# Optimization experiments

Hardware: AMD Instinct MI355X
Metric: run time of the kernel (lower is better)

## Reference

```python
import jax, jax.numpy as jnp
import numpy as np

NUM_HEADS = 16
D_K = 8  # == n_qubits


def setup_inputs() -> dict:
    key = jax.random.key(0)
    k1, k2, k3 = jax.random.split(key, 3)
    x = jax.random.normal(k1, (4, 2048, 128), dtype=jnp.float32)
    # trainable RX angles, one per qubit (tq.RX has_params=True)
    theta = jax.random.normal(k2, (D_K,), dtype=jnp.float32)
    # out_proj: Linear(embed_dim, embed_dim, bias=False)
    w_out = jax.random.normal(k3, (128, 128), dtype=jnp.float32) * (1.0 / np.sqrt(128.0))
    return {"x": x, "theta": theta, "w_out": w_out}


def quantum_features(x, theta):
    # x: [b, s, e]. Per head of size d_k: encode RX(x_i), trainable RX(theta_i)
    # (composes to RX(x_i + theta_i)), CNOT ladder [i, i+1], measure PauliZ.
    # Heisenberg picture: Z_w -> Z_0...Z_w, so <Z_w> = prod_{i<=w} cos(x_i + theta_i).
    b, s, e = x.shape
    heads = x.reshape(b, s, NUM_HEADS, D_K)
    return jnp.cumprod(jnp.cos(heads + theta), axis=-1)  # [b, s, h, d_k]


def reference(x, theta, w_out):
    b, s, e = x.shape
    # q == k == v: same shared q_layer applied to the same x three times.
    qkv = quantum_features(x, theta)            # [b, s, h, d_k]
    q = qkv.transpose(0, 2, 1, 3)               # [b, h, s, d_k]
    scores = jnp.einsum('bhqd,bhkd->bhqk', q, q) / np.sqrt(D_K)
    attn = jax.nn.softmax(scores, axis=-1)      # dropout is identity at eval
    out = jnp.einsum('bhqk,bhkd->bhqd', attn, q)
    out = out.transpose(0, 2, 1, 3).reshape(b, s, e)
    return out @ w_out.T
```

## Files before the change

kernel.cpp:

```cpp
#include <hip/hip_runtime.h>

#define BATCH 4
#define SEQ   2048
#define EMB   128
#define NH    16
#define DK    8

#define QSCALE 0.510069726f

typedef _Float16 v4h  __attribute__((ext_vector_type(4)));
typedef _Float16 v8h  __attribute__((ext_vector_type(8)));
typedef __fp16   v2fp __attribute__((ext_vector_type(2)));
typedef float    v4f  __attribute__((ext_vector_type(4)));
typedef float    v16f __attribute__((ext_vector_type(16)));

#define CHUNK  512
#define NCH    (SEQ / CHUNK)
#define VTP    520

__launch_bounds__(256, 4)
__global__ void attn_kernel(const float* __restrict__ x,
                            const float* __restrict__ theta,
                            _Float16* __restrict__ Ah ) {
  __shared__ __align__(16) _Float16 Kl[CHUNK * 8];
  __shared__ __align__(16) _Float16 VT[10][VTP];

  const int tid = threadIdx.x;
  const int L   = tid & 63;
  const int ln  = L & 31;
  const int hf  = L >> 5;
  const int wv  = tid >> 6;
  const int bh  = blockIdx.x >> 3;
  const int qg  = blockIdx.x & 7;
  const int b = bh >> 4;
  const int h = bh & 15;

  float th[DK];
#pragma unroll
  for (int i = 0; i < DK; ++i) th[i] = theta[i];

  for (int i = tid; i < VTP; i += 256) {
    VT[8][i] = (_Float16)1.0f;
    VT[9][i] = (_Float16)0.0f;
  }

  const int c0 = qg >> 1;
  const int mrow = (ln < 9) ? ln : 9;
  const float* xb = x + (size_t)b * SEQ * EMB + h * DK;

  float4 pa0, pa1, pb0, pb1;
  {
    const float* xp = xb + (size_t)(c0 * CHUNK + tid) * EMB;
    pa0 = *(const float4*)(xp);
    pa1 = *(const float4*)(xp + 4);
    pb0 = *(const float4*)(xp + 256 * EMB);
    pb1 = *(const float4*)(xp + 256 * EMB + 4);
  }

  v8h qf0 = {0, 0, 0, 0, 0, 0, 0, 0};
  v8h qf1 = {0, 0, 0, 0, 0, 0, 0, 0};
  v16f acc0, acc1, zf;
#pragma unroll
  for (int i = 0; i < 16; ++i) { acc0[i] = 0.f; acc1[i] = 0.f; zf[i] = 0.f; }

  for (int cc = 0; cc < NCH; ++cc) {
    if (cc) __syncthreads();

    {
      float r0[8], r1[8];
      r0[0] = __cosf(pa0.x + th[0]);
      r0[1] = r0[0] * __cosf(pa0.y + th[1]);
      r0[2] = r0[1] * __cosf(pa0.z + th[2]);
      r0[3] = r0[2] * __cosf(pa0.w + th[3]);
      r0[4] = r0[3] * __cosf(pa1.x + th[4]);
      r0[5] = r0[4] * __cosf(pa1.y + th[5]);
      r0[6] = r0[5] * __cosf(pa1.z + th[6]);
      r0[7] = r0[6] * __cosf(pa1.w + th[7]);
      r1[0] = __cosf(pb0.x + th[0]);
      r1[1] = r1[0] * __cosf(pb0.y + th[1]);
      r1[2] = r1[1] * __cosf(pb0.z + th[2]);
      r1[3] = r1[2] * __cosf(pb0.w + th[3]);
      r1[4] = r1[3] * __cosf(pb1.x + th[4]);
      r1[5] = r1[4] * __cosf(pb1.y + th[5]);
      r1[6] = r1[5] * __cosf(pb1.z + th[6]);
      r1[7] = r1[6] * __cosf(pb1.w + th[7]);

      _Float16 h0[8], h1[8];
#pragma unroll
      for (int i = 0; i < 8; ++i) { h0[i] = (_Float16)r0[i]; h1[i] = (_Float16)r1[i]; }

      union { v4h v[2]; float4 f; } u0, u1;
      u0.v[0] = (v4h){h0[0], h0[1], h0[2], h0[3]};
      u0.v[1] = (v4h){h0[4], h0[5], h0[6], h0[7]};
      u1.v[0] = (v4h){h1[0], h1[1], h1[2], h1[3]};
      u1.v[1] = (v4h){h1[4], h1[5], h1[6], h1[7]};
      *(float4*)&Kl[tid * 8]         = u0.f;
      *(float4*)&Kl[(tid + 256) * 8] = u1.f;

      const int j0 = tid, j1 = tid + 256;
      const int col0 = (j0 & ~15) | (j0 & 3) | ((j0 & 4) << 1) | ((j0 & 8) >> 1);
      const int col1 = (j1 & ~15) | (j1 & 3) | ((j1 & 4) << 1) | ((j1 & 8) >> 1);
#pragma unroll
      for (int d = 0; d < 8; ++d) {
        VT[d][col0] = h0[d];
        VT[d][col1] = h1[d];
      }
    }
    __syncthreads();

    if (cc + 1 < NCH) {
      const int cn = (c0 + cc + 1) & (NCH - 1);
      const float* xp = xb + (size_t)(cn * CHUNK + tid) * EMB;
      pa0 = *(const float4*)(xp);
      pa1 = *(const float4*)(xp + 4);
      pb0 = *(const float4*)(xp + 256 * EMB);
      pb1 = *(const float4*)(xp + 256 * EMB + 4);
    }

    if (cc == 0 && hf == 0) {
      const int ql = (qg & 1) * 256 + wv * 64 + ln;
      const _Float16 qs = (_Float16)QSCALE;
      const v8h qsc = {qs, qs, qs, qs, qs, qs, qs, qs};
      qf0 = *(const v8h*)&Kl[ql * 8] * qsc;
      qf1 = *(const v8h*)&Kl[(ql + 32) * 8] * qsc;
    }

    v8h kf = *(const v8h*)&Kl[ln * 8];
#pragma unroll 2
    for (int kb = 0; kb < CHUNK / 32; ++kb) {
      const v8h kf_n = *(const v8h*)&Kl[((((kb + 1) & 15) * 32) + ln) * 8];
      const v16f s0 = __builtin_amdgcn_mfma_f32_32x32x16_f16(kf, qf0, zf, 0, 0, 0);
      const v16f s1 = __builtin_amdgcn_mfma_f32_32x32x16_f16(kf, qf1, zf, 0, 0, 0);
      const v8h vt0 = *(const v8h*)&VT[mrow][kb * 32 + hf * 8];
      const v8h vt1 = *(const v8h*)&VT[mrow][kb * 32 + 16 + hf * 8];
      union { v2fp p[4]; v8h v; } a0, a1, b0, b1;
#pragma unroll
      for (int i = 0; i < 4; ++i) {
        a0.p[i] = __builtin_amdgcn_cvt_pkrtz(
            __builtin_amdgcn_exp2f(s0[2 * i]),
            __builtin_amdgcn_exp2f(s0[2 * i + 1]));
        a1.p[i] = __builtin_amdgcn_cvt_pkrtz(
            __builtin_amdgcn_exp2f(s0[8 + 2 * i]),
            __builtin_amdgcn_exp2f(s0[8 + 2 * i + 1]));
      }
      acc0 = __builtin_amdgcn_mfma_f32_32x32x16_f16(vt0, a0.v, acc0, 0, 0, 0);
      acc0 = __builtin_amdgcn_mfma_f32_32x32x16_f16(vt1, a1.v, acc0, 0, 0, 0);
#pragma unroll
      for (int i = 0; i < 4; ++i) {
        b0.p[i] = __builtin_amdgcn_cvt_pkrtz(
            __builtin_amdgcn_exp2f(s1[2 * i]),
            __builtin_amdgcn_exp2f(s1[2 * i + 1]));
        b1.p[i] = __builtin_amdgcn_cvt_pkrtz(
            __builtin_amdgcn_exp2f(s1[8 + 2 * i]),
            __builtin_amdgcn_exp2f(s1[8 + 2 * i + 1]));
      }
      acc1 = __builtin_amdgcn_mfma_f32_32x32x16_f16(vt0, b0.v, acc1, 0, 0, 0);
      acc1 = __builtin_amdgcn_mfma_f32_32x32x16_f16(vt1, b1.v, acc1, 0, 0, 0);
      kf = kf_n;
    }
  }

  {
    const int qrow0 = qg * 256 + wv * 64 + ln;
    const float den0 = __shfl(acc0[4], ln, 64);
    const float inv0 = 1.0f / den0;
    v4h o0 = {(_Float16)(acc0[0] * inv0), (_Float16)(acc0[1] * inv0),
              (_Float16)(acc0[2] * inv0), (_Float16)(acc0[3] * inv0)};
    *(v4h*)(Ah + ((size_t)b * SEQ + qrow0) * EMB + h * DK + hf * 4) = o0;

    const float den1 = __shfl(acc1[4], ln, 64);
    const float inv1 = 1.0f / den1;
    v4h o1 = {(_Float16)(acc1[0] * inv1), (_Float16)(acc1[1] * inv1),
              (_Float16)(acc1[2] * inv1), (_Float16)(acc1[3] * inv1)};
    *(v4h*)(Ah + ((size_t)b * SEQ + qrow0 + 32) * EMB + h * DK + hf * 4) = o1;
  }
}

__launch_bounds__(256, 4)
__global__ void proj_kernel(const _Float16* __restrict__ Ah,
                            const float* __restrict__ W,
                            float* __restrict__ out) {
  __shared__ __align__(16) _Float16 Ahs[32][136];
  __shared__ __align__(16) _Float16 Whs[64][136];

  const int tid  = threadIdx.x;
  const int L    = tid & 63;
  const int wv   = tid >> 6;
  const int quad = L >> 4;
  const int ln   = L & 15;
  const int rowbase = blockIdx.x * 32;
  const int colbase = blockIdx.y * 64;

#pragma unroll
  for (int it = 0; it < 2; ++it) {
    const int idx = it * 256 + tid;
    const int r  = idx >> 4;
    const int c8 = idx & 15;
    *(uint4*)&Ahs[r][c8 * 8] =
        *(const uint4*)(Ah + (size_t)(rowbase + r) * EMB + c8 * 8);
  }
#pragma unroll
  for (int it = 0; it < 8; ++it) {
    const int idx = it * 256 + tid;
    const int n  = idx >> 5;
    const int c4 = idx & 31;
    const float4 w = *(const float4*)(W + (size_t)(colbase + n) * EMB + c4 * 4);
    v4h wh = {(_Float16)w.x, (_Float16)w.y, (_Float16)w.z, (_Float16)w.w};
    *(v4h*)&Whs[n][c4 * 4] = wh;
  }
  __syncthreads();

  const int rowoff = (wv & 1) * 16;
  const int coloff = (wv >> 1) * 32;

  v4f acc[2];
#pragma unroll
  for (int nt = 0; nt < 2; ++nt) acc[nt] = (v4f){0.f, 0.f, 0.f, 0.f};

#pragma unroll
  for (int k8 = 0; k8 < 8; ++k8) {
    const v4h af = *(const v4h*)&Ahs[rowoff + ln][k8 * 16 + quad * 4];
#pragma unroll
    for (int nt = 0; nt < 2; ++nt) {
      const v4h bf = *(const v4h*)&Whs[coloff + nt * 16 + ln][k8 * 16 + quad * 4];
      acc[nt] = __builtin_amdgcn_mfma_f32_16x16x16f16(af, bf, acc[nt], 0, 0, 0);
    }
  }

#pragma unroll
  for (int nt = 0; nt < 2; ++nt) {
    const int col = colbase + coloff + nt * 16 + ln;
#pragma unroll
    for (int r = 0; r < 4; ++r) {
      out[(size_t)(rowbase + rowoff + quad * 4 + r) * EMB + col] = acc[nt][r];
    }
  }
}

extern "C" void kernel_launch(void* const* d_in, const int* in_sizes, int n_in,
                              void* d_out, int out_size, void* d_ws, size_t ws_size,
                              hipStream_t stream) {
  const float* x     = (const float*)d_in[0];
  const float* theta = (const float*)d_in[1];
  const float* w_out = (const float*)d_in[2];
  float* out = (float*)d_out;

  _Float16* Ah = (_Float16*)d_ws;

  attn_kernel<<<dim3(512), dim3(256), 0, stream>>>(x, theta, Ah);

  proj_kernel<<<dim3((BATCH * SEQ) / 32, 2), dim3(256), 0, stream>>>(Ah, w_out, out);
}
```

Measured before the change: 93.72 us.

## Fuse output projection into attention kernel via last-block-done counters

Merges the attention and projection kernels into one launch. Each attention block bumps an atomic counter for its (batch, query-group) tile, and the 16th block to arrive loads W into shared memory and computes the 256x128 projection for those rows from the fp16 attention output in global memory. This removes the second launch and the gap between kernels, at the cost of a serialized projection tail in 32 blocks and extra fences and atomics. The counter reset done by block 0 at kernel start relies on it running before any other block finishes.

```diff
diff --git a/kernel.cpp b/kernel.cpp
--- a/kernel.cpp
+++ b/kernel.cpp
@@ -19,21 +19,29 @@
 #define VTP    520
 
 __launch_bounds__(256, 4)
-__global__ void attn_kernel(const float* __restrict__ x,
-                            const float* __restrict__ theta,
-                            _Float16* __restrict__ Ah ) {
-  __shared__ __align__(16) _Float16 Kl[CHUNK * 8];
-  __shared__ __align__(16) _Float16 VT[10][VTP];
+__global__ void attn_proj_kernel(const float* __restrict__ x,
+                                 const float* __restrict__ theta,
+                                 const float* __restrict__ W,
+                                 float* __restrict__ out,
+                                 _Float16* __restrict__ Ah ,
+                                 unsigned* __restrict__ cnt ) {
+  __shared__ __align__(16) char smem[34816];
+  __shared__ int s_old;
+  _Float16* Kl = (_Float16*)smem;
+  _Float16 (*VT)[VTP] = (_Float16 (*)[VTP])(smem + 8192);
 
   const int tid = threadIdx.x;
   const int L   = tid & 63;
   const int ln  = L & 31;
   const int hf  = L >> 5;
   const int wv  = tid >> 6;
-  const int bh  = blockIdx.x >> 3;
-  const int qg  = blockIdx.x & 7;
+  const int bid = blockIdx.x;
+  const int bh  = bid >> 3;
+  const int qg  = bid & 7;
   const int b = bh >> 4;
   const int h = bh & 15;
+
+  if (bid == 0 && tid < 32) atomicExch(&cnt[tid], 0u);
 
   float th[DK];
 #pragma unroll
@@ -174,65 +182,52 @@
               (_Float16)(acc1[2] * inv1), (_Float16)(acc1[3] * inv1)};
     *(v4h*)(Ah + ((size_t)b * SEQ + qrow0 + 32) * EMB + h * DK + hf * 4) = o1;
   }
-}
-
-__launch_bounds__(256, 4)
-__global__ void proj_kernel(const _Float16* __restrict__ Ah,
-                            const float* __restrict__ W,
-                            float* __restrict__ out) {
-  __shared__ __align__(16) _Float16 Ahs[32][136];
-  __shared__ __align__(16) _Float16 Whs[64][136];
-
-  const int tid  = threadIdx.x;
-  const int L    = tid & 63;
-  const int wv   = tid >> 6;
-  const int quad = L >> 4;
-  const int ln   = L & 15;
-  const int rowbase = blockIdx.x * 32;
-  const int colbase = blockIdx.y * 64;
-
-#pragma unroll
-  for (int it = 0; it < 2; ++it) {
-    const int idx = it * 256 + tid;
-    const int r  = idx >> 4;
-    const int c8 = idx & 15;
-    *(uint4*)&Ahs[r][c8 * 8] =
-        *(const uint4*)(Ah + (size_t)(rowbase + r) * EMB + c8 * 8);
-  }
-#pragma unroll
-  for (int it = 0; it < 8; ++it) {
-    const int idx = it * 256 + tid;
-    const int n  = idx >> 5;
-    const int c4 = idx & 31;
-    const float4 w = *(const float4*)(W + (size_t)(colbase + n) * EMB + c4 * 4);
-    v4h wh = {(_Float16)w.x, (_Float16)w.y, (_Float16)w.z, (_Float16)w.w};
-    *(v4h*)&Whs[n][c4 * 4] = wh;
-  }
+
+  __threadfence();
   __syncthreads();
-
-  const int rowoff = (wv & 1) * 16;
-  const int coloff = (wv >> 1) * 32;
-
-  v4f acc[2];
-#pragma unroll
-  for (int nt = 0; nt < 2; ++nt) acc[nt] = (v4f){0.f, 0.f, 0.f, 0.f};
-
-#pragma unroll
-  for (int k8 = 0; k8 < 8; ++k8) {
-    const v4h af = *(const v4h*)&Ahs[rowoff + ln][k8 * 16 + quad * 4];
-#pragma unroll
-    for (int nt = 0; nt < 2; ++nt) {
-      const v4h bf = *(const v4h*)&Whs[coloff + nt * 16 + ln][k8 * 16 + quad * 4];
-      acc[nt] = __builtin_amdgcn_mfma_f32_16x16x16f16(af, bf, acc[nt], 0, 0, 0);
-    }
-  }
-
-#pragma unroll
-  for (int nt = 0; nt < 2; ++nt) {
-    const int col = colbase + coloff + nt * 16 + ln;
-#pragma unroll
-    for (int r = 0; r < 4; ++r) {
-      out[(size_t)(rowbase + rowoff + quad * 4 + r) * EMB + col] = acc[nt][r];
+  if (tid == 0) s_old = (int)atomicAdd(&cnt[b * 8 + qg], 1u);
+  __syncthreads();
+  if (s_old != 15) return;
+
+  __threadfence();
+  {
+    _Float16 (*Whs)[136] = (_Float16 (*)[136])smem;
+    __syncthreads();
+
+#pragma unroll
+    for (int it = 0; it < 16; ++it) {
+      const int idx = it * 256 + tid;
+      const int n  = idx >> 5;
+      const int c4 = idx & 31;
+      const float4 w = *(const float4*)(W + (size_t)n * EMB + c4 * 4);
+      v4h wh = {(_Float16)w.x, (_Float16)w.y, (_Float16)w.z, (_Float16)w.w};
+      *(v4h*)&Whs[n][c4 * 4] = wh;
+    }
+    __syncthreads();
+
+    const int quad = L >> 4;
+    const int l16  = L & 15;
+    const int coloff = wv * 32;
+    const size_t R0 = (size_t)b * SEQ + qg * 256;
+
+#pragma unroll 2
+    for (int rt = 0; rt < 16; ++rt) {
+      v4f pacc0 = (v4f){0.f, 0.f, 0.f, 0.f};
+      v4f pacc1 = (v4f){0.f, 0.f, 0.f, 0.f};
+#pragma unroll
+      for (int k8 = 0; k8 < 8; ++k8) {
+        const v4h af = *(const v4h*)(Ah + (R0 + rt * 16 + l16) * EMB
+                                        + k8 * 16 + quad * 4);
+        const v4h bf0 = *(const v4h*)&Whs[coloff + l16][k8 * 16 + quad * 4];
+        const v4h bf1 = *(const v4h*)&Whs[coloff + 16 + l16][k8 * 16 + quad * 4];
+        pacc0 = __builtin_amdgcn_mfma_f32_16x16x16f16(af, bf0, pacc0, 0, 0, 0);
+        pacc1 = __builtin_amdgcn_mfma_f32_16x16x16f16(af, bf1, pacc1, 0, 0, 0);
+      }
+#pragma unroll
+      for (int r = 0; r < 4; ++r) {
+        out[(R0 + rt * 16 + quad * 4 + r) * EMB + coloff + l16]      = pacc0[r];
+        out[(R0 + rt * 16 + quad * 4 + r) * EMB + coloff + 16 + l16] = pacc1[r];
+      }
     }
   }
 }
@@ -245,9 +240,9 @@
   const float* w_out = (const float*)d_in[2];
   float* out = (float*)d_out;
 
-  _Float16* Ah = (_Float16*)d_ws;
-
-  attn_kernel<<<dim3(512), dim3(256), 0, stream>>>(x, theta, Ah);
-
-  proj_kernel<<<dim3((BATCH * SEQ) / 32, 2), dim3(256), 0, stream>>>(Ah, w_out, out);
+  _Float16* Ah  = (_Float16*)d_ws;
+  unsigned* cnt = (unsigned*)(Ah + (size_t)BATCH * SEQ * EMB);
+
+  attn_proj_kernel<<<dim3(512), dim3(256), 0, stream>>>(x, theta, w_out, out,
+                                                        Ah, cnt);
 }
```

After: 177.8 us. 89.7% more time.

## Split key range across wave pairs, give each wave four query tiles

Applied to the files above, without the earlier changes.

Each wave now handles four 32-row query tiles instead of two and only half of each key chunk. Wave pairs split the key blocks, and their partial numerators and denominators are combined through shared memory at the end. The aim is to reuse each K/V fragment load across more MFMAs and to interleave the score MFMAs with the exp work. In exchange it raises register pressure (the launch bound drops to 2 blocks per CU) and adds a final shared-memory reduction with an extra barrier.

```diff
diff --git a/kernel.cpp b/kernel.cpp
--- a/kernel.cpp
+++ b/kernel.cpp
@@ -18,18 +18,21 @@
 #define NCH    (SEQ / CHUNK)
 #define VTP    520
 
-__launch_bounds__(256, 4)
+__launch_bounds__(256, 2)
 __global__ void attn_kernel(const float* __restrict__ x,
                             const float* __restrict__ theta,
                             _Float16* __restrict__ Ah ) {
-  __shared__ __align__(16) _Float16 Kl[CHUNK * 8];
-  __shared__ __align__(16) _Float16 VT[10][VTP];
+  __shared__ __align__(16) char smem[20480];
+  _Float16* Kl = (_Float16*)smem;
+  _Float16 (*VT)[VTP] = (_Float16 (*)[VTP])(smem + 8192);
 
   const int tid = threadIdx.x;
   const int L   = tid & 63;
   const int ln  = L & 31;
   const int hf  = L >> 5;
   const int wv  = tid >> 6;
+  const int kh  = wv & 1;
+  const int qq  = wv >> 1;
   const int bh  = blockIdx.x >> 3;
   const int qg  = blockIdx.x & 7;
   const int b = bh >> 4;
@@ -59,9 +62,13 @@
 
   v8h qf0 = {0, 0, 0, 0, 0, 0, 0, 0};
   v8h qf1 = {0, 0, 0, 0, 0, 0, 0, 0};
-  v16f acc0, acc1, zf;
-#pragma unroll
-  for (int i = 0; i < 16; ++i) { acc0[i] = 0.f; acc1[i] = 0.f; zf[i] = 0.f; }
+  v8h qf2 = {0, 0, 0, 0, 0, 0, 0, 0};
+  v8h qf3 = {0, 0, 0, 0, 0, 0, 0, 0};
+  v16f acc0, acc1, acc2, acc3, zf;
+#pragma unroll
+  for (int i = 0; i < 16; ++i) {
+    acc0[i] = 0.f; acc1[i] = 0.f; acc2[i] = 0.f; acc3[i] = 0.f; zf[i] = 0.f;
+  }
 
   for (int cc = 0; cc < NCH; ++cc) {
     if (cc) __syncthreads();
@@ -118,61 +125,102 @@
     }
 
     if (cc == 0 && hf == 0) {
-      const int ql = (qg & 1) * 256 + wv * 64 + ln;
+      const int qloc = (qg & 1) * 256 + qq * 128 + ln;
       const _Float16 qs = (_Float16)QSCALE;
       const v8h qsc = {qs, qs, qs, qs, qs, qs, qs, qs};
-      qf0 = *(const v8h*)&Kl[ql * 8] * qsc;
-      qf1 = *(const v8h*)&Kl[(ql + 32) * 8] * qsc;
-    }
-
-    v8h kf = *(const v8h*)&Kl[ln * 8];
+      qf0 = *(const v8h*)&Kl[(qloc)      * 8] * qsc;
+      qf1 = *(const v8h*)&Kl[(qloc + 32) * 8] * qsc;
+      qf2 = *(const v8h*)&Kl[(qloc + 64) * 8] * qsc;
+      qf3 = *(const v8h*)&Kl[(qloc + 96) * 8] * qsc;
+    }
+
+    const int tb = kh * 8;
+    v8h kf = *(const v8h*)&Kl[((tb)*32 + ln) * 8];
 #pragma unroll 2
-    for (int kb = 0; kb < CHUNK / 32; ++kb) {
-      const v8h kf_n = *(const v8h*)&Kl[((((kb + 1) & 15) * 32) + ln) * 8];
-      const v16f s0 = __builtin_amdgcn_mfma_f32_32x32x16_f16(kf, qf0, zf, 0, 0, 0);
-      const v16f s1 = __builtin_amdgcn_mfma_f32_32x32x16_f16(kf, qf1, zf, 0, 0, 0);
-      const v8h vt0 = *(const v8h*)&VT[mrow][kb * 32 + hf * 8];
-      const v8h vt1 = *(const v8h*)&VT[mrow][kb * 32 + 16 + hf * 8];
-      union { v2fp p[4]; v8h v; } a0, a1, b0, b1;
+    for (int kb = 0; kb < 8; ++kb) {
+      const int t = tb + kb;
+      const v8h kf_n = *(const v8h*)&Kl[((tb + ((kb + 1) & 7)) * 32 + ln) * 8];
+      const v8h vt0 = *(const v8h*)&VT[mrow][t * 32 + hf * 8];
+      const v8h vt1 = *(const v8h*)&VT[mrow][t * 32 + 16 + hf * 8];
+      v16f s_a = __builtin_amdgcn_mfma_f32_32x32x16_f16(kf, qf0, zf, 0, 0, 0);
+      v16f s_b = __builtin_amdgcn_mfma_f32_32x32x16_f16(kf, qf1, zf, 0, 0, 0);
+      union { v2fp p[4]; v8h v; } p0, p1;
 #pragma unroll
       for (int i = 0; i < 4; ++i) {
-        a0.p[i] = __builtin_amdgcn_cvt_pkrtz(
-            __builtin_amdgcn_exp2f(s0[2 * i]),
-            __builtin_amdgcn_exp2f(s0[2 * i + 1]));
-        a1.p[i] = __builtin_amdgcn_cvt_pkrtz(
-            __builtin_amdgcn_exp2f(s0[8 + 2 * i]),
-            __builtin_amdgcn_exp2f(s0[8 + 2 * i + 1]));
-      }
-      acc0 = __builtin_amdgcn_mfma_f32_32x32x16_f16(vt0, a0.v, acc0, 0, 0, 0);
-      acc0 = __builtin_amdgcn_mfma_f32_32x32x16_f16(vt1, a1.v, acc0, 0, 0, 0);
+        p0.p[i] = __builtin_amdgcn_cvt_pkrtz(
+            __builtin_amdgcn_exp2f(s_a[2 * i]),
+            __builtin_amdgcn_exp2f(s_a[2 * i + 1]));
+        p1.p[i] = __builtin_amdgcn_cvt_pkrtz(
+            __builtin_amdgcn_exp2f(s_a[8 + 2 * i]),
+            __builtin_amdgcn_exp2f(s_a[8 + 2 * i + 1]));
+      }
+      acc0 = __builtin_amdgcn_mfma_f32_32x32x16_f16(vt0, p0.v, acc0, 0, 0, 0);
+      acc0 = __builtin_amdgcn_mfma_f32_32x32x16_f16(vt1, p1.v, acc0, 0, 0, 0);
+      s_a = __builtin_amdgcn_mfma_f32_32x32x16_f16(kf, qf2, zf, 0, 0, 0);
 #pragma unroll
       for (int i = 0; i < 4; ++i) {
-        b0.p[i] = __builtin_amdgcn_cvt_pkrtz(
-            __builtin_amdgcn_exp2f(s1[2 * i]),
-            __builtin_amdgcn_exp2f(s1[2 * i + 1]));
-        b1.p[i] = __builtin_amdgcn_cvt_pkrtz(
-            __builtin_amdgcn_exp2f(s1[8 + 2 * i]),
-            __builtin_amdgcn_exp2f(s1[8 + 2 * i + 1]));
-      }
-      acc1 = __builtin_amdgcn_mfma_f32_32x32x16_f16(vt0, b0.v, acc1, 0, 0, 0);
-      acc1 = __builtin_amdgcn_mfma_f32_32x32x16_f16(vt1, b1.v, acc1, 0, 0, 0);
+        p0.p[i] = __builtin_amdgcn_cvt_pkrtz(
+            __builtin_amdgcn_exp2f(s_b[2 * i]),
+            __builtin_amdgcn_exp2f(s_b[2 * i + 1]));
+        p1.p[i] = __builtin_amdgcn_cvt_pkrtz(
+            __builtin_amdgcn_exp2f(s_b[8 + 2 * i]),
+            __builtin_amdgcn_exp2f(s_b[8 + 2 * i + 1]));
+      }
+      acc1 = __builtin_amdgcn_mfma_f32_32x32x16_f16(vt0, p0.v, acc1, 0, 0, 0);
+      acc1 = __builtin_amdgcn_mfma_f32_32x32x16_f16(vt1, p1.v, acc1, 0, 0, 0);
+      s_b = __builtin_amdgcn_mfma_f32_32x32x16_f16(kf, qf3, zf, 0, 0, 0);
+#pragma unroll
+      for (int i = 0; i < 4; ++i) {
+        p0.p[i] = __builtin_amdgcn_cvt_pkrtz(
+            __builtin_amdgcn_exp2f(s_a[2 * i]),
+            __builtin_amdgcn_exp2f(s_a[2 * i + 1]));
+        p1.p[i] = __builtin_amdgcn_cvt_pkrtz(
+            __builtin_amdgcn_exp2f(s_a[8 + 2 * i]),
+            __builtin_amdgcn_exp2f(s_a[8 + 2 * i + 1]));
+      }
+      acc2 = __builtin_amdgcn_mfma_f32_32x32x16_f16(vt0, p0.v, acc2, 0, 0, 0);
+      acc2 = __builtin_amdgcn_mfma_f32_32x32x16_f16(vt1, p1.v, acc2, 0, 0, 0);
+#pragma unroll
+      for (int i = 0; i < 4; ++i) {
+        p0.p[i] = __builtin_amdgcn_cvt_pkrtz(
+            __builtin_amdgcn_exp2f(s_b[2 * i]),
+            __builtin_amdgcn_exp2f(s_b[2 * i + 1]));
+        p1.p[i] = __builtin_amdgcn_cvt_pkrtz(
+            __builtin_amdgcn_exp2f(s_b[8 + 2 * i]),
+            __builtin_amdgcn_exp2f(s_b[8 + 2 * i + 1]));
+      }
+      acc3 = __builtin_amdgcn_mfma_f32_32x32x16_f16(vt0, p0.v, acc3, 0, 0, 0);
+      acc3 = __builtin_amdgcn_mfma_f32_32x32x16_f16(vt1, p1.v, acc3, 0, 0, 0);
       kf = kf_n;
     }
   }
 
+  __syncthreads();
   {
-    const int qrow0 = qg * 256 + wv * 64 + ln;
-    const float den0 = __shfl(acc0[4], ln, 64);
-    const float inv0 = 1.0f / den0;
-    v4h o0 = {(_Float16)(acc0[0] * inv0), (_Float16)(acc0[1] * inv0),
-              (_Float16)(acc0[2] * inv0), (_Float16)(acc0[3] * inv0)};
-    *(v4h*)(Ah + ((size_t)b * SEQ + qrow0) * EMB + h * DK + hf * 4) = o0;
-
-    const float den1 = __shfl(acc1[4], ln, 64);
-    const float inv1 = 1.0f / den1;
-    v4h o1 = {(_Float16)(acc1[0] * inv1), (_Float16)(acc1[1] * inv1),
-              (_Float16)(acc1[2] * inv1), (_Float16)(acc1[3] * inv1)};
-    *(v4h*)(Ah + ((size_t)b * SEQ + qrow0 + 32) * EMB + h * DK + hf * 4) = o1;
+    float (*P)[4][5][64] = (float (*)[4][5][64])smem;
+#pragma unroll
+    for (int r = 0; r < 5; ++r) {
+      P[wv][0][r][L] = acc0[r];
+      P[wv][1][r][L] = acc1[r];
+      P[wv][2][r][L] = acc2[r];
+      P[wv][3][r][L] = acc3[r];
+    }
+    __syncthreads();
+    const int q2 = qq * 2;
+#pragma unroll
+    for (int j = 0; j < 2; ++j) {
+      const int c = kh * 2 + j;
+      float sum[4];
+#pragma unroll
+      for (int r = 0; r < 4; ++r)
+        sum[r] = P[q2][c][r][L] + P[q2 + 1][c][r][L];
+      const float den = P[q2][c][4][ln] + P[q2 + 1][c][4][ln];
+      const float inv = 1.0f / den;
+      const int qrow = qg * 256 + (qq * 4 + c) * 32 + ln;
+      v4h o = {(_Float16)(sum[0] * inv), (_Float16)(sum[1] * inv),
+               (_Float16)(sum[2] * inv), (_Float16)(sum[3] * inv)};
+      *(v4h*)(Ah + ((size_t)b * SEQ + qrow) * EMB + h * DK + hf * 4) = o;
+    }
   }
 }
 
```

Measured after the change: 94.33 us. No clear change (+0.6%).
